# Kernel optimization log

Hardware: AMD Instinct MI355X
Metric: run time of the kernel (lower is better)

The kernel has to match this reference:

```python
import jax, jax.numpy as jnp
import numpy as np

H = 512
B = 64
S = 2048
NUM_LAYERS = 1


def setup_inputs() -> dict:
    key = jax.random.key(0)
    ks = jax.random.split(key, 8)
    scale = 1.0 / np.sqrt(H)
    return {
        "hidden": jax.random.normal(ks[0], (NUM_LAYERS, B, H), dtype=jnp.float32),
        "encoder_outputs": jax.random.normal(ks[1], (B, S, H), dtype=jnp.float32),
        "U_w": jax.random.uniform(ks[2], (H, H), jnp.float32, -scale, scale),
        "U_b": jax.random.uniform(ks[3], (H,), jnp.float32, -scale, scale),
        "W_w": jax.random.uniform(ks[4], (H, H), jnp.float32, -scale, scale),
        "W_b": jax.random.uniform(ks[5], (H,), jnp.float32, -scale, scale),
        "V_w": jax.random.uniform(ks[6], (1, H), jnp.float32, -scale, scale),
        "V_b": jax.random.uniform(ks[7], (1,), jnp.float32, -scale, scale),
    }


def reference(hidden, encoder_outputs, U_w, U_b, W_w, W_b, V_w, V_b):
    # hidden: [L, B, H] -> take last layer, like hidden[-1]
    h = hidden[-1]  # [B, H]
    # Uatt(h): [B, H] -> broadcast over src_len
    u = h @ U_w.T + U_b            # [B, H]
    w = jnp.einsum('bsh,kh->bsk', encoder_outputs, W_w) + W_b  # [B, S, H]
    combined = jnp.tanh(u[:, None, :] + w)                     # [B, S, H]
    energy = jnp.einsum('bsh,h->bs', combined, V_w[0]) + V_b[0]  # [B, S]
    attn = jax.nn.softmax(energy, axis=1)                       # [B, S]
    context = jnp.einsum('bs,bsh->bh', attn, encoder_outputs)   # [B, H]
    return (context, attn)
```

## Files before the change

kernel.cpp:

```cpp
#include <hip/hip_runtime.h>
#include <hip/hip_bf16.h>

#define H 512
#define B 64
#define S 2048

#define BM 128
#define BN 128
#define BK 32

typedef __bf16 bf16x8 __attribute__((ext_vector_type(8)));
typedef float f32x4 __attribute__((ext_vector_type(4)));

__device__ __forceinline__ unsigned cvt2(float x, float y) {
    union { __hip_bfloat162 h; unsigned u; } cv;
    cv.h = __float22bfloat162_rn(make_float2(x, y));
    return cv.u;
}

__device__ __forceinline__ float fast_tanh(float x) {
    float e = __expf(2.0f * x);
    float r = __builtin_amdgcn_rcpf(e + 1.0f);
    return 1.0f - 2.0f * r;
}

__global__ __launch_bounds__(256) void u_kernel(
        const float* __restrict__ hid, const float* __restrict__ Uw,
        const float* __restrict__ Ub, const float* __restrict__ Wb,
        float* __restrict__ u) {
    const int b = blockIdx.y;
    const int k = blockIdx.x * 4 + (threadIdx.x >> 6);
    const int lane = threadIdx.x & 63;
    const float4* wrow = (const float4*)(Uw + (size_t)k * H);
    const float4* hrow = (const float4*)(hid + (size_t)b * H);
    float4 w0 = wrow[lane * 2], w1 = wrow[lane * 2 + 1];
    float4 h0 = hrow[lane * 2], h1 = hrow[lane * 2 + 1];
    float acc = w0.x * h0.x + w0.y * h0.y + w0.z * h0.z + w0.w * h0.w
              + w1.x * h1.x + w1.y * h1.y + w1.z * h1.z + w1.w * h1.w;
    #pragma unroll
    for (int off = 1; off < 64; off <<= 1) acc += __shfl_xor(acc, off, 64);
    if (lane == 0) u[b * H + k] = acc + Ub[k] + Wb[k];
}

__global__ __launch_bounds__(256) void energy_kernel(
        const float* __restrict__ enc, const float* __restrict__ Ww,
        const float* __restrict__ Vw, const float* __restrict__ u,
        float* __restrict__ energy) {
    const int st = blockIdx.x;
    const int b  = blockIdx.y;
    const int s0 = st * BM;
    const int tid  = threadIdx.x;
    const int wave = tid >> 6;
    const int lane = tid & 63;
    const int wr = wave >> 1, wc = wave & 1;
    const int quad = lane >> 4, c = lane & 15;

    __shared__ unsigned short As[BM][BK];
    __shared__ unsigned short Bs[BN][BK];
    __shared__ float uS[H], vS[H];
    __shared__ float red[BM];

    #pragma unroll
    for (int i = tid; i < H; i += 256) { uS[i] = u[b * H + i]; vS[i] = Vw[i]; }

    const int srow = tid >> 3;
    const int sc4  = (tid & 7) * 4;
    const float* pA = enc + ((size_t)(b * S + s0) + srow) * H + sc4;

    float esum[4][4] = {};

    for (int kt = 0; kt < 4; ++kt) {
        const float* pB = Ww + ((size_t)(kt * BN) + srow) * H + sc4;
        f32x4 acc[4][4] = {};

        float4 pa[4], pb[4];
        #pragma unroll
        for (int i = 0; i < 4; ++i) {
            pa[i] = *(const float4*)(pA + (size_t)i * 32 * H);
            pb[i] = *(const float4*)(pB + (size_t)i * 32 * H);
        }

        for (int kk = 0; kk < H / BK; ++kk) {
            uint2 ap[4], bp[4];
            #pragma unroll
            for (int i = 0; i < 4; ++i) {
                ap[i].x = cvt2(pa[i].x, pa[i].y); ap[i].y = cvt2(pa[i].z, pa[i].w);
                bp[i].x = cvt2(pb[i].x, pb[i].y); bp[i].y = cvt2(pb[i].z, pb[i].w);
            }
            __syncthreads();
            #pragma unroll
            for (int i = 0; i < 4; ++i) {
                *(uint2*)&As[srow + i * 32][sc4] = ap[i];
                *(uint2*)&Bs[srow + i * 32][sc4] = bp[i];
            }
            __syncthreads();
            if (kk < H / BK - 1) {
                const int h0 = (kk + 1) * BK;
                #pragma unroll
                for (int i = 0; i < 4; ++i) {
                    pa[i] = *(const float4*)(pA + (size_t)i * 32 * H + h0);
                    pb[i] = *(const float4*)(pB + (size_t)i * 32 * H + h0);
                }
            }
            bf16x8 af[4], bfr[4];
            #pragma unroll
            for (int i = 0; i < 4; ++i) af[i]  = *(const bf16x8*)&As[wr * 64 + i * 16 + c][quad * 8];
            #pragma unroll
            for (int j = 0; j < 4; ++j) bfr[j] = *(const bf16x8*)&Bs[wc * 64 + j * 16 + c][quad * 8];
            #pragma unroll
            for (int i = 0; i < 4; ++i)
                #pragma unroll
                for (int j = 0; j < 4; ++j)
                    acc[i][j] = __builtin_amdgcn_mfma_f32_16x16x32_bf16(af[i], bfr[j], acc[i][j], 0, 0, 0);
        }

        #pragma unroll
        for (int i = 0; i < 4; ++i)
            #pragma unroll
            for (int j = 0; j < 4; ++j) {
                const int col = kt * BN + wc * 64 + j * 16 + c;
                const float v = vS[col], uu = uS[col];
                #pragma unroll
                for (int r = 0; r < 4; ++r)
                    esum[i][r] += v * fast_tanh(uu + acc[i][j][r]);
            }
    }

    #pragma unroll
    for (int i = 0; i < 4; ++i)
        #pragma unroll
        for (int r = 0; r < 4; ++r) {
            float e = esum[i][r];
            e += __shfl_xor(e, 1, 64);
            e += __shfl_xor(e, 2, 64);
            e += __shfl_xor(e, 4, 64);
            e += __shfl_xor(e, 8, 64);
            esum[i][r] = e;
        }
    __syncthreads();
    if (wc == 0 && c == 0) {
        #pragma unroll
        for (int i = 0; i < 4; ++i)
            #pragma unroll
            for (int r = 0; r < 4; ++r)
                red[wr * 64 + i * 16 + quad * 4 + r] = esum[i][r];
    }
    __syncthreads();
    if (wc == 1 && c == 0) {
        #pragma unroll
        for (int i = 0; i < 4; ++i)
            #pragma unroll
            for (int r = 0; r < 4; ++r) {
                const int row = wr * 64 + i * 16 + quad * 4 + r;
                energy[b * S + s0 + row] = red[row] + esum[i][r];
            }
    }
}

__global__ void softmax_kernel(const float* __restrict__ energy, float* __restrict__ attn) {
    int b = blockIdx.x;
    int t = threadIdx.x;
    const float* e = energy + b * S;
    float v[8];
    float m = -1e30f;
    #pragma unroll
    for (int i = 0; i < 8; ++i) { v[i] = e[t + i * 256]; m = fmaxf(m, v[i]); }
    #pragma unroll
    for (int off = 1; off < 64; off <<= 1) m = fmaxf(m, __shfl_xor(m, off, 64));
    __shared__ float redm[4], reds[4];
    if ((t & 63) == 0) redm[t >> 6] = m;
    __syncthreads();
    m = fmaxf(fmaxf(redm[0], redm[1]), fmaxf(redm[2], redm[3]));
    float s = 0.f;
    #pragma unroll
    for (int i = 0; i < 8; ++i) { v[i] = __expf(v[i] - m); s += v[i]; }
    #pragma unroll
    for (int off = 1; off < 64; off <<= 1) s += __shfl_xor(s, off, 64);
    if ((t & 63) == 0) reds[t >> 6] = s;
    __syncthreads();
    float inv = 1.0f / (reds[0] + reds[1] + reds[2] + reds[3]);
    #pragma unroll
    for (int i = 0; i < 8; ++i) attn[b * S + t + i * 256] = v[i] * inv;
}

#define CCHUNK 128
__global__ __launch_bounds__(256) void context_kernel(
        const float* __restrict__ enc, const float* __restrict__ attn,
        float* __restrict__ ctx) {
    int b  = blockIdx.x >> 4;
    int ch = blockIdx.x & 15;
    int t  = threadIdx.x;
    __shared__ float aS[CCHUNK];
    if (t < CCHUNK) aS[t] = attn[b * S + ch * CCHUNK + t];
    __syncthreads();
    const float* ebase = enc + ((size_t)(b * S + ch * CCHUNK)) * H + t;
    float c0 = 0.f, c1 = 0.f;
    #pragma unroll 8
    for (int s = 0; s < CCHUNK; ++s) {
        float a = aS[s];
        c0 += a * ebase[(size_t)s * H];
        c1 += a * ebase[(size_t)s * H + 256];
    }
    atomicAdd(&ctx[b * H + t], c0);
    atomicAdd(&ctx[b * H + t + 256], c1);
}

extern "C" void kernel_launch(void* const* d_in, const int* in_sizes, int n_in,
                              void* d_out, int out_size, void* d_ws, size_t ws_size,
                              hipStream_t stream) {
    (void)in_sizes; (void)n_in; (void)out_size; (void)ws_size;
    const float* hid = (const float*)d_in[0];
    const float* enc = (const float*)d_in[1];
    const float* Uw  = (const float*)d_in[2];
    const float* Ub  = (const float*)d_in[3];
    const float* Ww  = (const float*)d_in[4];
    const float* Wb  = (const float*)d_in[5];
    const float* Vw  = (const float*)d_in[6];

    float* out_ctx  = (float*)d_out;
    float* out_attn = out_ctx + B * H;
    float* energy   = (float*)d_ws;
    float* u        = energy + B * S;

    hipMemsetAsync(d_out, 0, (size_t)B * H * sizeof(float), stream);

    u_kernel<<<dim3(H / 4, B), 256, 0, stream>>>(hid, Uw, Ub, Wb, u);
    energy_kernel<<<dim3(S / BM, B), 256, 0, stream>>>(enc, Ww, Vw, u, energy);
    softmax_kernel<<<B, 256, 0, stream>>>(energy, out_attn);
    context_kernel<<<B * (S / CCHUNK), 256, 0, stream>>>(enc, out_attn, out_ctx);
}
```

Baseline: 549.5 us.

## Pre-convert encoder outputs to bf16 and load GEMM tiles directly to LDS

Adds a conversion pass that writes encoder_outputs and W_w to bf16 in workspace. The energy GEMM then streams tiles into shared memory with global_load_lds and no per-iteration register conversion, and the context reduction reads the bf16 copy at half the bytes. The full fp32 tensor is still read once and a 128MB bf16 copy is written, so traffic shifts rather than disappears. Context now uses bf16 encoder values, which lowers precision, and the path falls back to fp32 kernels when the workspace is too small.

```diff
diff --git a/kernel.cpp b/kernel.cpp
--- a/kernel.cpp
+++ b/kernel.cpp
@@ -6,7 +6,6 @@
 #define S 2048
 
 #define BM 128
-#define BN 128
 #define BK 32
 
 typedef __bf16 bf16x8 __attribute__((ext_vector_type(8)));
@@ -24,13 +23,42 @@
     return 1.0f - 2.0f * r;
 }
 
+__device__ __forceinline__ void load_lds16(const void* g, void* l) {
+    __builtin_amdgcn_global_load_lds(
+        (const __attribute__((address_space(1))) unsigned int*)g,
+        (__attribute__((address_space(3))) unsigned int*)l, 16, 0, 0);
+}
+
+#define CVT_GRID 4096
+__global__ __launch_bounds__(256) void cvt_kernel(const float* __restrict__ src,
+                                                  __hip_bfloat16* __restrict__ dst) {
+    size_t i = (size_t)blockIdx.x * 256 + threadIdx.x;
+    const size_t stride = (size_t)CVT_GRID * 256;
+    #pragma unroll
+    for (int k = 0; k < 8; ++k, i += stride) {
+        size_t e = i * 8;
+        float4 a = *(const float4*)(src + e);
+        float4 b = *(const float4*)(src + e + 4);
+        uint4 p = make_uint4(cvt2(a.x, a.y), cvt2(a.z, a.w), cvt2(b.x, b.y), cvt2(b.z, b.w));
+        *(uint4*)(dst + e) = p;
+    }
+}
+
 __global__ __launch_bounds__(256) void u_kernel(
         const float* __restrict__ hid, const float* __restrict__ Uw,
         const float* __restrict__ Ub, const float* __restrict__ Wb,
-        float* __restrict__ u) {
+        float* __restrict__ u, const float* __restrict__ Ww,
+        __hip_bfloat16* __restrict__ Wwb) {
     const int b = blockIdx.y;
     const int k = blockIdx.x * 4 + (threadIdx.x >> 6);
     const int lane = threadIdx.x & 63;
+    if (Wwb != nullptr && b == 0) {
+        int base = (blockIdx.x * 256 + threadIdx.x) * 8;
+        float4 a = *(const float4*)(Ww + base);
+        float4 c = *(const float4*)(Ww + base + 4);
+        uint4 p = make_uint4(cvt2(a.x, a.y), cvt2(a.z, a.w), cvt2(c.x, c.y), cvt2(c.z, c.w));
+        *(uint4*)(Wwb + base) = p;
+    }
     const float4* wrow = (const float4*)(Uw + (size_t)k * H);
     const float4* hrow = (const float4*)(hid + (size_t)b * H);
     float4 w0 = wrow[lane * 2], w1 = wrow[lane * 2 + 1];
@@ -42,8 +70,8 @@
     if (lane == 0) u[b * H + k] = acc + Ub[k] + Wb[k];
 }
 
-__global__ __launch_bounds__(256) void energy_kernel(
-        const float* __restrict__ enc, const float* __restrict__ Ww,
+__global__ __launch_bounds__(256, 4) void energy_kernel(
+        const __hip_bfloat16* __restrict__ encb, const __hip_bfloat16* __restrict__ Wwb,
         const float* __restrict__ Vw, const float* __restrict__ u,
         float* __restrict__ energy) {
     const int st = blockIdx.x;
@@ -55,58 +83,43 @@
     const int wr = wave >> 1, wc = wave & 1;
     const int quad = lane >> 4, c = lane & 15;
 
-    __shared__ unsigned short As[BM][BK];
-    __shared__ unsigned short Bs[BN][BK];
+    __shared__ __hip_bfloat16 As[BM * BK];
+    __shared__ __hip_bfloat16 Bs[BM * BK];
     __shared__ float uS[H], vS[H];
     __shared__ float red[BM];
 
     #pragma unroll
     for (int i = tid; i < H; i += 256) { uS[i] = u[b * H + i]; vS[i] = Vw[i]; }
 
-    const int srow = tid >> 3;
-    const int sc4  = (tid & 7) * 4;
-    const float* pA = enc + ((size_t)(b * S + s0) + srow) * H + sc4;
+    const int arow  = lane >> 2;
+    const int acol  = (lane & 3) * 8;
+    const int lds0  = wave * 1024 + lane * 8;
+    const int lds1  = lds0 + 512;
+    const size_t ga0 = ((size_t)(b * S + s0) + wave * 32 + arow) * H + acol;
+    const size_t ga1 = ga0 + (size_t)16 * H;
 
     float esum[4][4] = {};
 
     for (int kt = 0; kt < 4; ++kt) {
-        const float* pB = Ww + ((size_t)(kt * BN) + srow) * H + sc4;
+        const size_t gb0 = ((size_t)(kt * BM) + wave * 32 + arow) * H + acol;
+        const size_t gb1 = gb0 + (size_t)16 * H;
         f32x4 acc[4][4] = {};
 
-        float4 pa[4], pb[4];
-        #pragma unroll
-        for (int i = 0; i < 4; ++i) {
-            pa[i] = *(const float4*)(pA + (size_t)i * 32 * H);
-            pb[i] = *(const float4*)(pB + (size_t)i * 32 * H);
-        }
-
         for (int kk = 0; kk < H / BK; ++kk) {
-            uint2 ap[4], bp[4];
-            #pragma unroll
-            for (int i = 0; i < 4; ++i) {
-                ap[i].x = cvt2(pa[i].x, pa[i].y); ap[i].y = cvt2(pa[i].z, pa[i].w);
-                bp[i].x = cvt2(pb[i].x, pb[i].y); bp[i].y = cvt2(pb[i].z, pb[i].w);
-            }
+            const int h0 = kk * BK;
             __syncthreads();
-            #pragma unroll
-            for (int i = 0; i < 4; ++i) {
-                *(uint2*)&As[srow + i * 32][sc4] = ap[i];
-                *(uint2*)&Bs[srow + i * 32][sc4] = bp[i];
-            }
+            load_lds16(encb + ga0 + h0, &As[lds0]);
+            load_lds16(encb + ga1 + h0, &As[lds1]);
+            load_lds16(Wwb + gb0 + h0, &Bs[lds0]);
+            load_lds16(Wwb + gb1 + h0, &Bs[lds1]);
             __syncthreads();
-            if (kk < H / BK - 1) {
-                const int h0 = (kk + 1) * BK;
-                #pragma unroll
-                for (int i = 0; i < 4; ++i) {
-                    pa[i] = *(const float4*)(pA + (size_t)i * 32 * H + h0);
-                    pb[i] = *(const float4*)(pB + (size_t)i * 32 * H + h0);
-                }
-            }
             bf16x8 af[4], bfr[4];
             #pragma unroll
-            for (int i = 0; i < 4; ++i) af[i]  = *(const bf16x8*)&As[wr * 64 + i * 16 + c][quad * 8];
-            #pragma unroll
-            for (int j = 0; j < 4; ++j) bfr[j] = *(const bf16x8*)&Bs[wc * 64 + j * 16 + c][quad * 8];
+            for (int i = 0; i < 4; ++i)
+                af[i] = *(const bf16x8*)&As[(wr * 64 + i * 16 + c) * BK + quad * 8];
+            #pragma unroll
+            for (int j = 0; j < 4; ++j)
+                bfr[j] = *(const bf16x8*)&Bs[(wc * 64 + j * 16 + c) * BK + quad * 8];
             #pragma unroll
             for (int i = 0; i < 4; ++i)
                 #pragma unroll
@@ -118,7 +131,7 @@
         for (int i = 0; i < 4; ++i)
             #pragma unroll
             for (int j = 0; j < 4; ++j) {
-                const int col = kt * BN + wc * 64 + j * 16 + c;
+                const int col = kt * BM + wc * 64 + j * 16 + c;
                 const float v = vS[col], uu = uS[col];
                 #pragma unroll
                 for (int r = 0; r < 4; ++r)
@@ -157,12 +170,89 @@
     }
 }
 
+__global__ __launch_bounds__(256) void energy_f32_kernel(
+        const float* __restrict__ enc, const float* __restrict__ Ww,
+        const float* __restrict__ Vw, const float* __restrict__ u,
+        float* __restrict__ energy) {
+    const int st = blockIdx.x, b = blockIdx.y;
+    const int s0 = st * BM;
+    const int tid = threadIdx.x, wave = tid >> 6, lane = tid & 63;
+    const int wr = wave >> 1, wc = wave & 1, quad = lane >> 4, c = lane & 15;
+    __shared__ unsigned short As[BM][BK];
+    __shared__ unsigned short Bs[BM][BK];
+    __shared__ float uS[H], vS[H], red[BM];
+    for (int i = tid; i < H; i += 256) { uS[i] = u[b * H + i]; vS[i] = Vw[i]; }
+    const int srow = tid >> 3, sc4 = (tid & 7) * 4;
+    const float* pA = enc + ((size_t)(b * S + s0) + srow) * H + sc4;
+    float esum[4][4] = {};
+    for (int kt = 0; kt < 4; ++kt) {
+        const float* pB = Ww + ((size_t)(kt * BM) + srow) * H + sc4;
+        f32x4 acc[4][4] = {};
+        for (int kk = 0; kk < H / BK; ++kk) {
+            const int h0 = kk * BK;
+            uint2 ap[4], bp[4];
+            #pragma unroll
+            for (int i = 0; i < 4; ++i) {
+                float4 a4 = *(const float4*)(pA + (size_t)i * 32 * H + h0);
+                float4 b4 = *(const float4*)(pB + (size_t)i * 32 * H + h0);
+                ap[i].x = cvt2(a4.x, a4.y); ap[i].y = cvt2(a4.z, a4.w);
+                bp[i].x = cvt2(b4.x, b4.y); bp[i].y = cvt2(b4.z, b4.w);
+            }
+            __syncthreads();
+            #pragma unroll
+            for (int i = 0; i < 4; ++i) {
+                *(uint2*)&As[srow + i * 32][sc4] = ap[i];
+                *(uint2*)&Bs[srow + i * 32][sc4] = bp[i];
+            }
+            __syncthreads();
+            bf16x8 af[4], bfr[4];
+            #pragma unroll
+            for (int i = 0; i < 4; ++i) af[i]  = *(const bf16x8*)&As[wr * 64 + i * 16 + c][quad * 8];
+            #pragma unroll
+            for (int j = 0; j < 4; ++j) bfr[j] = *(const bf16x8*)&Bs[wc * 64 + j * 16 + c][quad * 8];
+            #pragma unroll
+            for (int i = 0; i < 4; ++i)
+                #pragma unroll
+                for (int j = 0; j < 4; ++j)
+                    acc[i][j] = __builtin_amdgcn_mfma_f32_16x16x32_bf16(af[i], bfr[j], acc[i][j], 0, 0, 0);
+        }
+        #pragma unroll
+        for (int i = 0; i < 4; ++i)
+            #pragma unroll
+            for (int j = 0; j < 4; ++j) {
+                const int col = kt * BM + wc * 64 + j * 16 + c;
+                const float v = vS[col], uu = uS[col];
+                #pragma unroll
+                for (int r = 0; r < 4; ++r) esum[i][r] += v * fast_tanh(uu + acc[i][j][r]);
+            }
+    }
+    #pragma unroll
+    for (int i = 0; i < 4; ++i)
+        #pragma unroll
+        for (int r = 0; r < 4; ++r) {
+            float e = esum[i][r];
+            e += __shfl_xor(e, 1, 64); e += __shfl_xor(e, 2, 64);
+            e += __shfl_xor(e, 4, 64); e += __shfl_xor(e, 8, 64);
+            esum[i][r] = e;
+        }
+    __syncthreads();
+    if (wc == 0 && c == 0)
+        for (int i = 0; i < 4; ++i)
+            for (int r = 0; r < 4; ++r)
+                red[wr * 64 + i * 16 + quad * 4 + r] = esum[i][r];
+    __syncthreads();
+    if (wc == 1 && c == 0)
+        for (int i = 0; i < 4; ++i)
+            for (int r = 0; r < 4; ++r) {
+                const int row = wr * 64 + i * 16 + quad * 4 + r;
+                energy[b * S + s0 + row] = red[row] + esum[i][r];
+            }
+}
+
 __global__ void softmax_kernel(const float* __restrict__ energy, float* __restrict__ attn) {
-    int b = blockIdx.x;
-    int t = threadIdx.x;
+    int b = blockIdx.x, t = threadIdx.x;
     const float* e = energy + b * S;
-    float v[8];
-    float m = -1e30f;
+    float v[8]; float m = -1e30f;
     #pragma unroll
     for (int i = 0; i < 8; ++i) { v[i] = e[t + i * 256]; m = fmaxf(m, v[i]); }
     #pragma unroll
@@ -183,20 +273,47 @@
     for (int i = 0; i < 8; ++i) attn[b * S + t + i * 256] = v[i] * inv;
 }
 
-#define CCHUNK 128
-__global__ __launch_bounds__(256) void context_kernel(
+__global__ __launch_bounds__(256) void context_bf16_kernel(
+        const __hip_bfloat16* __restrict__ encb, const float* __restrict__ attn,
+        float* __restrict__ ctx) {
+    const int b = blockIdx.x >> 4, ch = blockIdx.x & 15;
+    const int t = threadIdx.x;
+    const int col8 = (t & 63) * 8, rg = t >> 6;
+    __shared__ float aS[128];
+    __shared__ float part[4][H];
+    if (t < 128) aS[t] = attn[b * S + ch * 128 + t];
+    __syncthreads();
+    const size_t rbase = (size_t)(b * S + ch * 128) * H;
+    float c0[8] = {};
+    #pragma unroll 4
+    for (int i = 0; i < 32; ++i) {
+        int s = rg * 32 + i;
+        bf16x8 ev = *(const bf16x8*)(encb + rbase + (size_t)s * H + col8);
+        float a = aS[s];
+        #pragma unroll
+        for (int j = 0; j < 8; ++j) c0[j] += a * (float)ev[j];
+    }
+    #pragma unroll
+    for (int j = 0; j < 8; ++j) part[rg][col8 + j] = c0[j];
+    __syncthreads();
+    #pragma unroll
+    for (int j = 0; j < 2; ++j) {
+        int col = t * 2 + j;
+        atomicAdd(&ctx[b * H + col], part[0][col] + part[1][col] + part[2][col] + part[3][col]);
+    }
+}
+
+__global__ __launch_bounds__(256) void context_f32_kernel(
         const float* __restrict__ enc, const float* __restrict__ attn,
         float* __restrict__ ctx) {
-    int b  = blockIdx.x >> 4;
-    int ch = blockIdx.x & 15;
-    int t  = threadIdx.x;
-    __shared__ float aS[CCHUNK];
-    if (t < CCHUNK) aS[t] = attn[b * S + ch * CCHUNK + t];
-    __syncthreads();
-    const float* ebase = enc + ((size_t)(b * S + ch * CCHUNK)) * H + t;
+    int b = blockIdx.x >> 4, ch = blockIdx.x & 15, t = threadIdx.x;
+    __shared__ float aS[128];
+    if (t < 128) aS[t] = attn[b * S + ch * 128 + t];
+    __syncthreads();
+    const float* ebase = enc + ((size_t)(b * S + ch * 128)) * H + t;
     float c0 = 0.f, c1 = 0.f;
     #pragma unroll 8
-    for (int s = 0; s < CCHUNK; ++s) {
+    for (int s = 0; s < 128; ++s) {
         float a = aS[s];
         c0 += a * ebase[(size_t)s * H];
         c1 += a * ebase[(size_t)s * H + 256];
@@ -208,7 +325,7 @@
 extern "C" void kernel_launch(void* const* d_in, const int* in_sizes, int n_in,
                               void* d_out, int out_size, void* d_ws, size_t ws_size,
                               hipStream_t stream) {
-    (void)in_sizes; (void)n_in; (void)out_size; (void)ws_size;
+    (void)in_sizes; (void)n_in; (void)out_size;
     const float* hid = (const float*)d_in[0];
     const float* enc = (const float*)d_in[1];
     const float* Uw  = (const float*)d_in[2];
@@ -219,13 +336,26 @@
 
     float* out_ctx  = (float*)d_out;
     float* out_attn = out_ctx + B * H;
-    float* energy   = (float*)d_ws;
-    float* u        = energy + B * S;
+    char*  ws       = (char*)d_ws;
+    float* energy   = (float*)ws;
+    float* u        = (float*)(ws + 524288);
+    __hip_bfloat16* encb = (__hip_bfloat16*)(ws + 655360);
+    __hip_bfloat16* Wwb  = (__hip_bfloat16*)(ws + 655360 + 134217728);
+    const size_t need = 655360 + 134217728 + 524288;
+    const bool fast = ws_size >= need;
 
     hipMemsetAsync(d_out, 0, (size_t)B * H * sizeof(float), stream);
 
-    u_kernel<<<dim3(H / 4, B), 256, 0, stream>>>(hid, Uw, Ub, Wb, u);
-    energy_kernel<<<dim3(S / BM, B), 256, 0, stream>>>(enc, Ww, Vw, u, energy);
-    softmax_kernel<<<B, 256, 0, stream>>>(energy, out_attn);
-    context_kernel<<<B * (S / CCHUNK), 256, 0, stream>>>(enc, out_attn, out_ctx);
-}
+    if (fast) {
+        cvt_kernel<<<CVT_GRID, 256, 0, stream>>>(enc, encb);
+        u_kernel<<<dim3(H / 4, B), 256, 0, stream>>>(hid, Uw, Ub, Wb, u, Ww, Wwb);
+        energy_kernel<<<dim3(S / BM, B), 256, 0, stream>>>(encb, Wwb, Vw, u, energy);
+        softmax_kernel<<<B, 256, 0, stream>>>(energy, out_attn);
+        context_bf16_kernel<<<B * 16, 256, 0, stream>>>(encb, out_attn, out_ctx);
+    } else {
+        u_kernel<<<dim3(H / 4, B), 256, 0, stream>>>(hid, Uw, Ub, Wb, u, Ww, nullptr);
+        energy_f32_kernel<<<dim3(S / BM, B), 256, 0, stream>>>(enc, Ww, Vw, u, energy);
+        softmax_kernel<<<B, 256, 0, stream>>>(energy, out_attn);
+        context_f32_kernel<<<B * 16, 256, 0, stream>>>(enc, out_attn, out_ctx);
+    }
+}
```

Result: slower. 615.4 us (+12.0%).
